# Performance work log

Hardware: AMD Instinct MI355X
Metric: run time of the kernel (lower is better)

The kernel has to match this reference:

```python
import jax, jax.numpy as jnp
import numpy as np

BETA = 0.99  # EMA momentum from init_kwargs
EPS = 1e-12  # torch F.normalize eps


def _normalize(v):
    # matches torch.nn.functional.normalize (L2, dim=-1, eps clamp)
    n = jnp.maximum(jnp.linalg.norm(v, axis=-1, keepdims=True), EPS)
    return v / n


def setup_inputs() -> dict:
    key = jax.random.key(0)
    k1, k2 = jax.random.split(key)
    x = jax.random.normal(k1, (16384, 1024), dtype=jnp.float32)
    group_features = jax.random.uniform(k2, (8192, 1024), dtype=jnp.float32)
    return {"x": x, "group_features": group_features}


def reference(x, group_features):
    n_groups = group_features.shape[0]
    # assign_groups: cosine-sim argmax (normalized copies; does NOT modify x used below)
    xn = _normalize(x)
    gn = _normalize(group_features)
    logits = xn @ gn.T                      # [B, G]
    assignments = jnp.argmax(logits, axis=-1)  # [B] int

    # bincount over groups
    counts = jax.ops.segment_sum(
        jnp.ones_like(assignments, dtype=jnp.int32), assignments, num_segments=n_groups
    )  # [G]

    # scale only groups that received at least one sample by beta
    gf = jnp.where((counts > 0)[:, None], group_features * BETA, group_features)

    # scatter-add EMA contribution: (1-beta) * mean-style sum of raw x per group
    per_sample = x / counts[assignments][:, None].astype(x.dtype)  # safe: count>=1 for assigned
    contrib = jax.ops.segment_sum(per_sample, assignments, num_segments=n_groups)  # [G, D]
    gf = gf + (1.0 - BETA) * contrib

    return _normalize(gf)
```

## Files before the change

### kernel.cpp

```cpp
#include <hip/hip_runtime.h>

#define B_N 16384
#define G_N 8192
#define D_N 1024
#define NT 96

typedef unsigned short u16;
typedef unsigned long long u64;
typedef __attribute__((ext_vector_type(8))) short short8;
typedef __attribute__((ext_vector_type(16))) float f32x16;

#define AS1 __attribute__((address_space(1)))
#define AS3 __attribute__((address_space(3)))


__global__ __launch_bounds__(256) void k_norms(const float* __restrict__ g,
                                               float* __restrict__ invn) {
    const int j = blockIdx.x;
    const int t = threadIdx.x;
    const float4 v = *reinterpret_cast<const float4*>(&g[(size_t)j * D_N + t * 4]);
    float s = v.x * v.x + v.y * v.y + v.z * v.z + v.w * v.w;
#pragma unroll
    for (int off = 32; off >= 1; off >>= 1) s += __shfl_down(s, off, 64);
    __shared__ float wsum[4];
    if ((t & 63) == 0) wsum[t >> 6] = s;
    __syncthreads();
    if (t == 0) {
        const float tot = wsum[0] + wsum[1] + wsum[2] + wsum[3];
        invn[j] = 1.0f / fmaxf(sqrtf(tot), 1e-12f);
    }
}

__global__ void k_counts(const u64* __restrict__ pk, int* __restrict__ counts) {
    const int i = blockIdx.x * blockDim.x + threadIdx.x;
    if (i < B_N) {
        const int a = 8191 - (int)(pk[i] & 0x1FFFull);
        atomicAdd(&counts[a], 1);
    }
}

__global__ __launch_bounds__(256) void k_scatter(const float* __restrict__ x,
                                                 const u64* __restrict__ pk,
                                                 const int* __restrict__ counts,
                                                 float* __restrict__ contrib) {
    const int i = blockIdx.x;
    const int a = 8191 - (int)(pk[i] & 0x1FFFull);
    const float scale = 1.0f / (float)counts[a];
    const int t = threadIdx.x;
    const float4 v = *reinterpret_cast<const float4*>(&x[(size_t)i * D_N + t * 4]);
    float* dst = &contrib[(size_t)a * D_N + t * 4];
    atomicAdd(dst + 0, v.x * scale);
    atomicAdd(dst + 1, v.y * scale);
    atomicAdd(dst + 2, v.z * scale);
    atomicAdd(dst + 3, v.w * scale);
}

__global__ __launch_bounds__(256) void k_finalize(const float* __restrict__ g,
                                                  const int* __restrict__ counts,
                                                  float* __restrict__ out) {
    const int j = blockIdx.x;
    const int t = threadIdx.x;
    const float sc = (counts[j] > 0) ? 0.99f : 1.0f;
    const float4 gv = *reinterpret_cast<const float4*>(&g[(size_t)j * D_N + t * 4]);
    const float4 cv = *reinterpret_cast<const float4*>(&out[(size_t)j * D_N + t * 4]);
    float4 gf;
    gf.x = sc * gv.x + 0.01f * cv.x;
    gf.y = sc * gv.y + 0.01f * cv.y;
    gf.z = sc * gv.z + 0.01f * cv.z;
    gf.w = sc * gv.w + 0.01f * cv.w;
    float s = gf.x * gf.x + gf.y * gf.y + gf.z * gf.z + gf.w * gf.w;
#pragma unroll
    for (int off = 32; off >= 1; off >>= 1) s += __shfl_down(s, off, 64);
    __shared__ float wsum[4];
    __shared__ float s_inv;
    if ((t & 63) == 0) wsum[t >> 6] = s;
    __syncthreads();
    if (t == 0) s_inv = 1.0f / fmaxf(sqrtf(wsum[0] + wsum[1] + wsum[2] + wsum[3]), 1e-12f);
    __syncthreads();
    gf.x *= s_inv; gf.y *= s_inv; gf.z *= s_inv; gf.w *= s_inv;
    *reinterpret_cast<float4*>(&out[(size_t)j * D_N + t * 4]) = gf;
}


__device__ inline u16 f2bf_rtn(float f) {
    unsigned u = __float_as_uint(f);
    unsigned r = u + 0x7fffu + ((u >> 16) & 1u);
    return (u16)(r >> 16);
}
__device__ inline float bf2f(u16 h) { return __uint_as_float(((unsigned)h) << 16); }

__global__ __launch_bounds__(256) void k_split_pack(const float* __restrict__ src,
                                                    u16* __restrict__ hi,
                                                    u16* __restrict__ lo) {
    const int id = blockIdx.x * 256 + threadIdx.x;
    const int brick = id >> 7, c = id & 127;
    const int mu = brick >> 5, tau = brick & 31;
    const int ks = c >> 6, lane = c & 63;
    const int row = mu * 32 + (lane & 31);
    const int k = tau * 32 + ks * 16 + (lane >> 5) * 8;
    const float* s = src + (size_t)row * D_N + k;
    const float4 v0 = *reinterpret_cast<const float4*>(s);
    const float4 v1 = *reinterpret_cast<const float4*>(s + 4);
    const float f[8] = {v0.x, v0.y, v0.z, v0.w, v1.x, v1.y, v1.z, v1.w};
    short8 h, l;
#pragma unroll
    for (int j = 0; j < 8; ++j) {
        const u16 hj = f2bf_rtn(f[j]);
        h[j] = (short)hj;
        l[j] = (short)f2bf_rtn(f[j] - bf2f(hj));
    }
    *reinterpret_cast<short8*>(hi + (size_t)id * 8) = h;
    *reinterpret_cast<short8*>(lo + (size_t)id * 8) = l;
}


#define MFMA_BLK(S) do {                                                                   \
    __builtin_amdgcn_s_setprio(1);                                                         \
    _Pragma("unroll")                                                                      \
    for (int ks = 0; ks < 2; ++ks)                                                         \
        _Pragma("unroll")                                                                  \
        for (int m = 0; m < 4; ++m)                                                        \
            _Pragma("unroll")                                                              \
            for (int n = 0; n < 2; ++n)                                                    \
                acc[m][n] = __builtin_amdgcn_mfma_f32_32x32x16_bf16(                       \
                    afr[S][m][ks], bfr[S][n][ks], acc[m][n], 0, 0, 0);                     \
    __builtin_amdgcn_s_setprio(0);                                                         \
} while (0)

#define READS(BUF, S) do {                                                                 \
    const u16* aB = lds + (BUF) * 16384 + aRd;                                             \
    const u16* bB = lds + (BUF) * 16384 + 8192 + bRd;                                      \
    _Pragma("unroll")                                                                      \
    for (int m = 0; m < 4; ++m)                                                            \
        _Pragma("unroll")                                                                  \
        for (int ks = 0; ks < 2; ++ks)                                                     \
            afr[S][m][ks] = *reinterpret_cast<const short8*>(aB + m * 1024 + ks * 512);    \
    _Pragma("unroll")                                                                      \
    for (int n = 0; n < 2; ++n)                                                            \
        _Pragma("unroll")                                                                  \
        for (int ks = 0; ks < 2; ++ks)                                                     \
            bfr[S][n][ks] = *reinterpret_cast<const short8*>(bB + n * 1024 + ks * 512);    \
} while (0)

#define BODY(P, BSTG, BRD, SM, SR) do {                                                    \
    asm volatile("s_waitcnt vmcnt(0)" ::: "memory");                                       \
    __builtin_amdgcn_s_barrier();                                                          \
    STG((P) + 2, BSTG);                                                                    \
    READS(BRD, SR);                                                                        \
    MFMA_BLK(SM);                                                                          \
} while (0)

__global__ __launch_bounds__(512, 2) void k_gemm_argmax(
    const u16* __restrict__ x_hi, const u16* __restrict__ x_lo,
    const u16* __restrict__ g_hi, const u16* __restrict__ g_lo,
    const float* __restrict__ invn, u64* __restrict__ pk) {

    __shared__ __align__(16) u16 lds[49152];

    const int bid = blockIdx.x;
    const int xcd = bid & 7, lcl = bid >> 3;
    const int mblk = xcd * 8 + ((lcl >> 3) & 7);
    const int nblk = (lcl & 7) + (lcl >> 6) * 8;
    const int mrow0 = mblk * 256, nrow0 = nblk * 256;

    const int tid = threadIdx.x;
    const int lane = tid & 63;
    const int w = tid >> 6;
    const int wr = w >> 2, wc = w & 3;
    const int l31 = lane & 31, l5 = lane >> 5;

    const int aRd = (wr * 512 + lane) * 8;
    const int bRd = (wc * 256 + lane) * 8;

    const int wub = (tid & 448) * 8;
    const int cOff = (tid & 127) * 8;
    const int brkA = tid >> 7;
    const size_t aBase = ((size_t)(mblk * 8 + brkA)) * 32768 + cOff;
    const size_t bBase = ((size_t)(nblk * 8 + brkA)) * 32768 + cOff;

    auto STG = [&](int T, int buf) {
        const int Tc = T < NT ? T : NT - 1;
        const int term = Tc >> 5;
        const int tko = (Tc & 31) * 1024;
        const u16* xa = ((term == 1) ? x_lo : x_hi) + aBase + tko;
        const u16* gb = ((term == 2) ? g_lo : g_hi) + bBase + tko;
        u16* da = lds + buf * 16384 + wub;
        u16* db = da + 8192;
        __builtin_amdgcn_global_load_lds((const AS1 void*)xa,            (AS3 void*)da, 16, 0, 0);
        __builtin_amdgcn_global_load_lds((const AS1 void*)(xa + 131072), (AS3 void*)(da + 4096), 16, 0, 0);
        __builtin_amdgcn_global_load_lds((const AS1 void*)gb,            (AS3 void*)db, 16, 0, 0);
        __builtin_amdgcn_global_load_lds((const AS1 void*)(gb + 131072), (AS3 void*)(db + 4096), 16, 0, 0);
    };

    f32x16 acc[4][2];
#pragma unroll
    for (int m = 0; m < 4; ++m)
#pragma unroll
        for (int n = 0; n < 2; ++n)
#pragma unroll
            for (int r = 0; r < 16; ++r) acc[m][n][r] = 0.0f;

    short8 afr[2][4][2], bfr[2][2][2];

    STG(0, 0); STG(1, 1);
    asm volatile("s_waitcnt vmcnt(4)" ::: "memory");
    __builtin_amdgcn_s_barrier();
    READS(0, 0);

    for (int it = 0; it < 16; ++it) {
        const int p = it * 6;
        BODY(p,     2, 1, 0, 1);
        BODY(p + 1, 0, 2, 1, 0);
        BODY(p + 2, 1, 0, 0, 1);
        BODY(p + 3, 2, 1, 1, 0);
        BODY(p + 4, 0, 2, 0, 1);
        BODY(p + 5, 1, 0, 1, 0);
    }

    float inv[2];
    inv[0] = invn[nrow0 + wc * 64 + l31];
    inv[1] = invn[nrow0 + wc * 64 + 32 + l31];

#pragma unroll
    for (int m = 0; m < 4; ++m) {
#pragma unroll
        for (int r = 0; r < 16; ++r) {
            u64 p = 0;
#pragma unroll
            for (int n = 0; n < 2; ++n) {
                const float v = acc[m][n][r] * inv[n];
                unsigned u = __float_as_uint(v);
                u ^= (u >> 31) ? 0xFFFFFFFFu : 0x80000000u;
                const int col = nrow0 + wc * 64 + n * 32 + l31;
                const u64 cand = ((u64)u << 13) | (unsigned)(8191 - col);
                p = (cand > p) ? cand : p;
            }
#pragma unroll
            for (int msk = 1; msk < 32; msk <<= 1) {
                const u64 o = __shfl_xor(p, msk, 64);
                p = (o > p) ? o : p;
            }
            if (l31 == 0) {
                const int row = mrow0 + wr * 128 + m * 32 + (r & 3) + 8 * (r >> 2) + 4 * l5;
                atomicMax(&pk[row], p);
            }
        }
    }
}


__global__ __launch_bounds__(256) void k_argmax_fp32(const float* __restrict__ x,
                                                     const float* __restrict__ g,
                                                     const float* __restrict__ invn,
                                                     int* __restrict__ assign) {
    __shared__ __align__(16) float As[32][68];
    __shared__ __align__(16) float Bs[32][68];
    const int t = threadIdx.x;
    const int tx = t & 15;
    const int ty = t >> 4;
    const int row0 = blockIdx.x * 64;
    const int r_a = t >> 3;
    const int c4 = t & 7;
    float bestv[4]; int besti[4];
#pragma unroll
    for (int i = 0; i < 4; ++i) { bestv[i] = -3.0e38f; besti[i] = 0; }
    for (int jt = 0; jt < G_N / 64; ++jt) {
        float acc[4][4] = {};
        for (int kt = 0; kt < D_N / 32; ++kt) {
#pragma unroll
            for (int p = 0; p < 2; ++p) {
                const int r = r_a + p * 32;
                const float4 va = *reinterpret_cast<const float4*>(&x[(size_t)(row0 + r) * D_N + kt * 32 + c4 * 4]);
                As[c4 * 4 + 0][r] = va.x; As[c4 * 4 + 1][r] = va.y; As[c4 * 4 + 2][r] = va.z; As[c4 * 4 + 3][r] = va.w;
                const float4 vb = *reinterpret_cast<const float4*>(&g[(size_t)(jt * 64 + r) * D_N + kt * 32 + c4 * 4]);
                Bs[c4 * 4 + 0][r] = vb.x; Bs[c4 * 4 + 1][r] = vb.y; Bs[c4 * 4 + 2][r] = vb.z; Bs[c4 * 4 + 3][r] = vb.w;
            }
            __syncthreads();
#pragma unroll
            for (int k = 0; k < 32; ++k) {
                const float4 a = *reinterpret_cast<const float4*>(&As[k][ty * 4]);
                const float4 b = *reinterpret_cast<const float4*>(&Bs[k][tx * 4]);
                const float av[4] = {a.x, a.y, a.z, a.w};
                const float bv[4] = {b.x, b.y, b.z, b.w};
#pragma unroll
                for (int i = 0; i < 4; ++i)
#pragma unroll
                    for (int jj = 0; jj < 4; ++jj) acc[i][jj] += av[i] * bv[jj];
            }
            __syncthreads();
        }
#pragma unroll
        for (int jj = 0; jj < 4; ++jj) {
            const int col = jt * 64 + tx * 4 + jj;
            const float s = invn[col];
#pragma unroll
            for (int i = 0; i < 4; ++i) {
                const float v = acc[i][jj] * s;
                if (v > bestv[i]) { bestv[i] = v; besti[i] = col; }
            }
        }
    }
#pragma unroll
    for (int m = 1; m < 16; m <<= 1) {
#pragma unroll
        for (int i = 0; i < 4; ++i) {
            const float ov = __shfl_xor(bestv[i], m, 64);
            const int oi = __shfl_xor(besti[i], m, 64);
            if (ov > bestv[i] || (ov == bestv[i] && oi < besti[i])) { bestv[i] = ov; besti[i] = oi; }
        }
    }
    if (tx == 0) {
#pragma unroll
        for (int i = 0; i < 4; ++i) assign[row0 + ty * 4 + i] = besti[i];
    }
}

__global__ void k_counts_i(const int* __restrict__ assign, int* __restrict__ counts) {
    const int i = blockIdx.x * blockDim.x + threadIdx.x;
    if (i < B_N) atomicAdd(&counts[assign[i]], 1);
}

__global__ __launch_bounds__(256) void k_scatter_i(const float* __restrict__ x,
                                                   const int* __restrict__ assign,
                                                   const int* __restrict__ counts,
                                                   float* __restrict__ contrib) {
    const int i = blockIdx.x;
    const int a = assign[i];
    const float scale = 1.0f / (float)counts[a];
    const int t = threadIdx.x;
    const float4 v = *reinterpret_cast<const float4*>(&x[(size_t)i * D_N + t * 4]);
    float* dst = &contrib[(size_t)a * D_N + t * 4];
    atomicAdd(dst + 0, v.x * scale);
    atomicAdd(dst + 1, v.y * scale);
    atomicAdd(dst + 2, v.z * scale);
    atomicAdd(dst + 3, v.w * scale);
}


extern "C" void kernel_launch(void* const* d_in, const int* in_sizes, int n_in,
                              void* d_out, int out_size, void* d_ws, size_t ws_size,
                              hipStream_t stream) {
    const float* x = (const float*)d_in[0];
    const float* g = (const float*)d_in[1];
    float* out = (float*)d_out;

    char* ws = (char*)d_ws;
    u16*  x_hi  = (u16*)(ws);
    u16*  x_lo  = (u16*)(ws + 33554432);
    u16*  g_hi  = (u16*)(ws + 67108864);
    u16*  g_lo  = (u16*)(ws + 83886080);
    float* invn = (float*)(ws + 100663296);
    int* counts = (int*)(ws + 100696064);
    u64*   pk   = (u64*)(ws + 100728832);
    const size_t need = 100859904;

    hipMemsetAsync(out, 0, (size_t)G_N * D_N * sizeof(float), stream);

    if (ws_size >= need) {
        hipMemsetAsync(counts, 0, (size_t)G_N * sizeof(int), stream);
        hipMemsetAsync(pk, 0, (size_t)B_N * sizeof(u64), stream);
        k_norms<<<G_N, 256, 0, stream>>>(g, invn);
        k_split_pack<<<B_N * D_N / 8 / 256, 256, 0, stream>>>(x, x_hi, x_lo);
        k_split_pack<<<G_N * D_N / 8 / 256, 256, 0, stream>>>(g, g_hi, g_lo);
        k_gemm_argmax<<<2048, 512, 0, stream>>>(x_hi, x_lo, g_hi, g_lo, invn, pk);
        k_counts<<<B_N / 256, 256, 0, stream>>>(pk, counts);
        k_scatter<<<B_N, 256, 0, stream>>>(x, pk, counts, out);
        k_finalize<<<G_N, 256, 0, stream>>>(g, counts, out);
    } else {
        float* invn_f = (float*)ws;
        int* assign_f = (int*)(ws + (size_t)G_N * 4);
        int* counts_f = (int*)(ws + (size_t)(G_N + B_N) * 4);
        hipMemsetAsync(counts_f, 0, (size_t)G_N * sizeof(int), stream);
        k_norms<<<G_N, 256, 0, stream>>>(g, invn_f);
        k_argmax_fp32<<<B_N / 64, 256, 0, stream>>>(x, g, invn_f, assign_f);
        k_counts_i<<<B_N / 256, 256, 0, stream>>>(assign_f, counts_f);
        k_scatter_i<<<B_N, 256, 0, stream>>>(x, assign_f, counts_f, out);
        k_finalize<<<G_N, 256, 0, stream>>>(g, counts_f, out);
    }
}
```

Baseline: 1.030 ms.

## Drop register double-buffering and relax global-load wait in GEMM main loop

Replaces the two-slot register fragment pipeline (LDS reads for the next step issued alongside MFMAs of the current step) with a single fragment set. Each step now reads from LDS and then runs its MFMAs. The global-to-LDS wait is loosened from vmcnt(0) to vmcnt(4), so one staged tile can stay in flight, and a second barrier is added per step. This cuts fragment register use and makes prefetch deeper. In exchange it loses the intra-wave overlap of LDS reads with MFMA, and the extra barrier adds synchronisation per step.

```diff
diff --git a/kernel.cpp b/kernel.cpp
--- a/kernel.cpp
+++ b/kernel.cpp
@@ -114,40 +114,41 @@
 }
 
 
-#define MFMA_BLK(S) do {                                                                   \
+#define MFMA_BLK() do {                                                                    \
     __builtin_amdgcn_s_setprio(1);                                                         \
-    _Pragma("unroll")                                                                      \
-    for (int ks = 0; ks < 2; ++ks)                                                         \
-        _Pragma("unroll")                                                                  \
-        for (int m = 0; m < 4; ++m)                                                        \
-            _Pragma("unroll")                                                              \
-            for (int n = 0; n < 2; ++n)                                                    \
-                acc[m][n] = __builtin_amdgcn_mfma_f32_32x32x16_bf16(                       \
-                    afr[S][m][ks], bfr[S][n][ks], acc[m][n], 0, 0, 0);                     \
-    __builtin_amdgcn_s_setprio(0);                                                         \
-} while (0)
-
-#define READS(BUF, S) do {                                                                 \
-    const u16* aB = lds + (BUF) * 16384 + aRd;                                             \
-    const u16* bB = lds + (BUF) * 16384 + 8192 + bRd;                                      \
     _Pragma("unroll")                                                                      \
     for (int m = 0; m < 4; ++m)                                                            \
         _Pragma("unroll")                                                                  \
         for (int ks = 0; ks < 2; ++ks)                                                     \
-            afr[S][m][ks] = *reinterpret_cast<const short8*>(aB + m * 1024 + ks * 512);    \
+            _Pragma("unroll")                                                              \
+            for (int n = 0; n < 2; ++n)                                                    \
+                acc[m][n] = __builtin_amdgcn_mfma_f32_32x32x16_bf16(                       \
+                    afr[m][ks], bfr[n][ks], acc[m][n], 0, 0, 0);                           \
+    __builtin_amdgcn_s_setprio(0);                                                         \
+} while (0)
+
+#define READS(BUF) do {                                                                    \
+    const u16* aB = lds + (BUF) * 16384 + aRd;                                             \
+    const u16* bB = lds + (BUF) * 16384 + 8192 + bRd;                                      \
     _Pragma("unroll")                                                                      \
     for (int n = 0; n < 2; ++n)                                                            \
         _Pragma("unroll")                                                                  \
         for (int ks = 0; ks < 2; ++ks)                                                     \
-            bfr[S][n][ks] = *reinterpret_cast<const short8*>(bB + n * 1024 + ks * 512);    \
+            bfr[n][ks] = *reinterpret_cast<const short8*>(bB + n * 1024 + ks * 512);       \
+    _Pragma("unroll")                                                                      \
+    for (int m = 0; m < 4; ++m)                                                            \
+        _Pragma("unroll")                                                                  \
+        for (int ks = 0; ks < 2; ++ks)                                                     \
+            afr[m][ks] = *reinterpret_cast<const short8*>(aB + m * 1024 + ks * 512);       \
 } while (0)
 
-#define BODY(P, BSTG, BRD, SM, SR) do {                                                    \
-    asm volatile("s_waitcnt vmcnt(0)" ::: "memory");                                       \
+#define BODY(P, BSTG, BRD) do {                                                            \
+    STG((P) + 2, BSTG);                                                                    \
+    READS(BRD);                                                                            \
     __builtin_amdgcn_s_barrier();                                                          \
-    STG((P) + 2, BSTG);                                                                    \
-    READS(BRD, SR);                                                                        \
-    MFMA_BLK(SM);                                                                          \
+    MFMA_BLK();                                                                            \
+    asm volatile("s_waitcnt vmcnt(4)" ::: "memory");                                       \
+    __builtin_amdgcn_s_barrier();                                                          \
 } while (0)
 
 __global__ __launch_bounds__(512, 2) void k_gemm_argmax(
@@ -200,21 +201,17 @@
 #pragma unroll
             for (int r = 0; r < 16; ++r) acc[m][n][r] = 0.0f;
 
-    short8 afr[2][4][2], bfr[2][2][2];
+    short8 afr[4][2], bfr[2][2];
 
     STG(0, 0); STG(1, 1);
     asm volatile("s_waitcnt vmcnt(4)" ::: "memory");
     __builtin_amdgcn_s_barrier();
-    READS(0, 0);
-
-    for (int it = 0; it < 16; ++it) {
-        const int p = it * 6;
-        BODY(p,     2, 1, 0, 1);
-        BODY(p + 1, 0, 2, 1, 0);
-        BODY(p + 2, 1, 0, 0, 1);
-        BODY(p + 3, 2, 1, 1, 0);
-        BODY(p + 4, 0, 2, 0, 1);
-        BODY(p + 5, 1, 0, 1, 0);
+
+    for (int it = 0; it < 32; ++it) {
+        const int q = it * 3;
+        BODY(q,     2, 0);
+        BODY(q + 1, 0, 1);
+        BODY(q + 2, 1, 2);
     }
 
     float inv[2];
```

Result: no change. 1.037 ms (+0.7%).
